# Kernel tuning notes

Hardware: AMD Instinct MI355X
Metric: run time of the kernel (lower is better)

The kernel has to match this reference:

```python
import math
import jax, jax.numpy as jnp
import numpy as np

B, Q, K = 1, 2048, 2048
CQ = CK = CV = 128
H, CH = 8, 32
HD = H * CH  # 256


def setup_inputs() -> dict:
    key = jax.random.key(0)
    ks = jax.random.split(key, 12)
    s = 0.02
    return {
        "q_x": jax.random.normal(ks[0], (B, Q, CQ), jnp.float32),
        "kv_x": jax.random.normal(ks[1], (B, K, CK), jnp.float32),
        "bias": jax.random.normal(ks[2], (B, 1, Q, K), jnp.float32),
        "distance": jax.random.uniform(ks[3], (B, Q, K, H), jnp.float32),
        "Wq": jax.random.normal(ks[4], (CQ, HD), jnp.float32) * s,
        "Wk": jax.random.normal(ks[5], (CK, HD), jnp.float32) * s,
        "Wv": jax.random.normal(ks[6], (CV, HD), jnp.float32) * s,
        "Wg": jax.random.normal(ks[7], (CQ, HD), jnp.float32) * s,
        "bg": jnp.zeros((HD,), jnp.float32),
        "Wo": jax.random.normal(ks[8], (HD, CQ), jnp.float32) * s,
        "bo": jnp.zeros((CQ,), jnp.float32),
    }


def reference(q_x, kv_x, bias, distance, Wq, Wk, Wv, Wg, bg, Wo, bo):
    # Projections -> [B, S, H, CH]
    q = (q_x @ Wq).reshape(B, Q, H, CH) / math.sqrt(CH)
    k = (kv_x @ Wk).reshape(B, K, H, CH)
    v = (kv_x @ Wv).reshape(B, K, H, CH)
    # Scores [B, H, Q, K]
    a = jnp.einsum("bqhc,bkhc->bhqk", q, k)
    a = a + bias
    # mha_permu=True: distance [B,Q,K,H] -> [B,H,Q,K]; rel_dis_pair_bias='add'
    a = a + jnp.transpose(distance, (0, 3, 1, 2))
    a = jax.nn.softmax(a, axis=-1)
    o = jnp.einsum("bhqk,bkhc->bqhc", a, v)  # [B, Q, H, CH]
    # Gating
    g = jax.nn.sigmoid(q_x @ Wg + bg).reshape(B, Q, H, CH)
    o = o * g
    o = o.reshape(B, Q, HD)
    return o @ Wo + bo
```

## Files before the change

### kernel.cpp

```cpp
#include <hip/hip_runtime.h>
#include <hip/hip_bf16.h>

#define Qn 2048
#define Kn 2048
#define Cin 128
#define Hn 8
#define CHn 32
#define HDn 256
#define QK (Qn * Kn)
#define NSPLIT 8

typedef __attribute__((ext_vector_type(8))) short short8;
typedef __attribute__((ext_vector_type(4))) float f32x4;

static __device__ __forceinline__ unsigned short f2bf(float f) {
    unsigned int u = __float_as_uint(f);
    u += 0x7fffu + ((u >> 16) & 1u);
    return (unsigned short)(u >> 16);
}

__global__ __launch_bounds__(256) void proj_kernel(
    const float* __restrict__ qx, const float* __restrict__ kvx,
    const float* __restrict__ Wq, const float* __restrict__ Wk,
    const float* __restrict__ Wv, const float* __restrict__ Wg,
    const float* __restrict__ bg,
    unsigned short* __restrict__ qb, unsigned short* __restrict__ kb,
    unsigned short* __restrict__ vtb, float* __restrict__ gb)
{
    const int mat = blockIdx.y;
    const int r0 = blockIdx.x * 8;
    const int j = threadIdx.x;
    const float* A = (mat == 0 || mat == 3) ? qx : kvx;
    const float* W = (mat == 0) ? Wq : (mat == 1) ? Wk : (mat == 2) ? Wv : Wg;
    const float* Ar = A + r0 * Cin;
    float acc[8] = {0.f, 0.f, 0.f, 0.f, 0.f, 0.f, 0.f, 0.f};
    for (int c = 0; c < Cin; ++c) {
        const float w = W[c * HDn + j];
        #pragma unroll
        for (int i = 0; i < 8; ++i)
            acc[i] = fmaf(Ar[i * Cin + c], w, acc[i]);
    }
    if (mat == 0) {
        const float s = 0.17677669529663687f;
        #pragma unroll
        for (int i = 0; i < 8; ++i)
            qb[(r0 + i) * HDn + j] = f2bf(acc[i] * s);
    } else if (mat == 1) {
        #pragma unroll
        for (int i = 0; i < 8; ++i)
            kb[(r0 + i) * HDn + j] = f2bf(acc[i]);
    } else if (mat == 2) {
        unsigned short tmp[8];
        #pragma unroll
        for (int i = 0; i < 8; ++i) tmp[i] = f2bf(acc[i]);
        *(short8*)(vtb + (size_t)j * Kn + r0) = *(short8*)tmp;
    } else {
        const float b = bg[j];
        #pragma unroll
        for (int i = 0; i < 8; ++i)
            gb[(r0 + i) * HDn + j] = 1.f / (1.f + __expf(-(acc[i] + b)));
    }
}

__global__ __launch_bounds__(256) void prepass_kernel(
    const float* __restrict__ bias, const float* __restrict__ dist,
    _Float16* __restrict__ db)
{
    __shared__ _Float16 lds[Hn * 272];
    const int q = blockIdx.x;
    const int k0 = blockIdx.y * 256;
    const int t = threadIdx.x;
    const float b = bias[q * Kn + k0 + t];
    const float4* dp = (const float4*)(dist + (size_t)(q * Kn + k0 + t) * Hn);
    const float4 d0 = dp[0];
    const float4 d1 = dp[1];
    lds[0 * 272 + t] = (_Float16)(d0.x + b);
    lds[1 * 272 + t] = (_Float16)(d0.y + b);
    lds[2 * 272 + t] = (_Float16)(d0.z + b);
    lds[3 * 272 + t] = (_Float16)(d0.w + b);
    lds[4 * 272 + t] = (_Float16)(d1.x + b);
    lds[5 * 272 + t] = (_Float16)(d1.y + b);
    lds[6 * 272 + t] = (_Float16)(d1.z + b);
    lds[7 * 272 + t] = (_Float16)(d1.w + b);
    __syncthreads();
    const int h = t >> 5;
    const int c8 = (t & 31) * 8;
    const short8 v = *(const short8*)(lds + h * 272 + c8);
    *(short8*)((unsigned short*)db + (size_t)h * QK + (size_t)q * Kn + k0 + c8) = v;
}

template <bool USE_DB>
__global__ __launch_bounds__(512) void attn_kernel(
    const unsigned short* __restrict__ qb, const unsigned short* __restrict__ kb,
    const unsigned short* __restrict__ vtb,
    const _Float16* __restrict__ db,
    const float* __restrict__ bias, const float* __restrict__ dist,
    float* __restrict__ opart, float* __restrict__ lpart)
{
    __shared__ unsigned short ps[Hn][16][72];
    const int bx = blockIdx.x;
    const int qt = bx >> 3;
    const int sp = bx & 7;
    const int q0 = qt * 16;
    const int k00 = sp * 256;
    const int tid = threadIdx.x;
    const int h = tid >> 6;
    const int l = tid & 63;
    const int g = l >> 4;
    const int n = l & 15;

    const short8 qf = *(const short8*)(qb + (q0 + n) * HDn + h * CHn + g * 8);
    const _Float16* dbh = db + (size_t)h * QK;

    f32x4 o0 = {0.f, 0.f, 0.f, 0.f};
    f32x4 o1 = {0.f, 0.f, 0.f, 0.f};
    float lacc[4] = {0.f, 0.f, 0.f, 0.f};
    unsigned short* psh = &ps[h][0][0];
    const f32x4 z = {0.f, 0.f, 0.f, 0.f};

    for (int kt = 0; kt < 4; ++kt) {
        const int k0 = k00 + kt * 64;
        float dbv[4][4];
        #pragma unroll
        for (int kkg = 0; kkg < 4; ++kkg) {
            #pragma unroll
            for (int r = 0; r < 4; ++r) {
                const int qg = q0 + g * 4 + r;
                const int kg = k0 + kkg * 16 + n;
                if (USE_DB)
                    dbv[kkg][r] = (float)dbh[(size_t)qg * Kn + kg];
                else
                    dbv[kkg][r] = bias[(size_t)qg * Kn + kg] +
                                  dist[((size_t)qg * Kn + kg) * Hn + h];
            }
        }
        f32x4 sf[4];
        #pragma unroll
        for (int kkg = 0; kkg < 4; ++kkg) {
            const short8 kf = *(const short8*)(kb + (k0 + kkg * 16 + n) * HDn + h * CHn + g * 8);
            sf[kkg] = __builtin_amdgcn_mfma_f32_16x16x32_bf16(qf, kf, z, 0, 0, 0);
        }
        #pragma unroll
        for (int kkg = 0; kkg < 4; ++kkg) {
            #pragma unroll
            for (int r = 0; r < 4; ++r) {
                const float p = __expf(sf[kkg][r] + dbv[kkg][r]);
                sf[kkg][r] = p;
                lacc[r] += p;
            }
        }
        #pragma unroll
        for (int kkg = 0; kkg < 4; ++kkg) {
            #pragma unroll
            for (int r = 0; r < 4; ++r)
                psh[(g * 4 + r) * 72 + kkg * 16 + n] = f2bf(sf[kkg][r]);
        }
        #pragma unroll
        for (int chunk = 0; chunk < 2; ++chunk) {
            const short8 pf = *(const short8*)(psh + n * 72 + chunk * 32 + g * 8);
            const short8 vf0 = *(const short8*)(vtb + (h * CHn + n) * Kn + k0 + chunk * 32 + g * 8);
            o0 = __builtin_amdgcn_mfma_f32_16x16x32_bf16(pf, vf0, o0, 0, 0, 0);
            const short8 vf1 = *(const short8*)(vtb + (h * CHn + 16 + n) * Kn + k0 + chunk * 32 + g * 8);
            o1 = __builtin_amdgcn_mfma_f32_16x16x32_bf16(pf, vf1, o1, 0, 0, 0);
        }
    }
    float* op = opart + (size_t)sp * (Qn * HDn);
    #pragma unroll
    for (int r = 0; r < 4; ++r) {
        const int qg = q0 + g * 4 + r;
        op[qg * HDn + h * CHn + n] = o0[r];
        op[qg * HDn + h * CHn + 16 + n] = o1[r];
        float v = lacc[r];
        v += __shfl_xor(v, 1);
        v += __shfl_xor(v, 2);
        v += __shfl_xor(v, 4);
        v += __shfl_xor(v, 8);
        lacc[r] = v;
    }
    if (n == 0) {
        float* lp = lpart + (size_t)sp * (Qn * Hn);
        #pragma unroll
        for (int r = 0; r < 4; ++r)
            lp[(q0 + g * 4 + r) * Hn + h] = lacc[r];
    }
}

__global__ __launch_bounds__(256) void mergeout_kernel(
    const float* __restrict__ opart, const float* __restrict__ lpart,
    const float* __restrict__ gb, const float* __restrict__ Wo,
    const float* __restrict__ bo, float* __restrict__ out)
{
    __shared__ float olds[HDn];
    __shared__ float red[4][128];
    const int q = blockIdx.x;
    const int t = threadIdx.x;
    const int h = t >> 5;
    float s = 0.f;
    #pragma unroll
    for (int sp = 0; sp < NSPLIT; ++sp)
        s += opart[(size_t)sp * (Qn * HDn) + q * HDn + t];
    float lt = 0.f;
    #pragma unroll
    for (int sp = 0; sp < NSPLIT; ++sp)
        lt += lpart[(size_t)sp * (Qn * Hn) + q * Hn + h];
    olds[t] = (s / lt) * gb[q * HDn + t];
    __syncthreads();
    const int p = t & 63;
    const int seg = t >> 6;
    float a0 = 0.f, a1 = 0.f;
    for (int c = seg * 64; c < seg * 64 + 64; ++c) {
        const float ov = olds[c];
        const float2 w = *(const float2*)(Wo + c * Cin + 2 * p);
        a0 = fmaf(ov, w.x, a0);
        a1 = fmaf(ov, w.y, a1);
    }
    red[seg][2 * p] = a0;
    red[seg][2 * p + 1] = a1;
    __syncthreads();
    if (t < 128)
        out[q * Cin + t] = red[0][t] + red[1][t] + red[2][t] + red[3][t] + bo[t];
}

extern "C" void kernel_launch(void* const* d_in, const int* in_sizes, int n_in,
                              void* d_out, int out_size, void* d_ws, size_t ws_size,
                              hipStream_t stream)
{
    const float* qx   = (const float*)d_in[0];
    const float* kvx  = (const float*)d_in[1];
    const float* bias = (const float*)d_in[2];
    const float* dist = (const float*)d_in[3];
    const float* Wq   = (const float*)d_in[4];
    const float* Wk   = (const float*)d_in[5];
    const float* Wv   = (const float*)d_in[6];
    const float* Wg   = (const float*)d_in[7];
    const float* bg   = (const float*)d_in[8];
    const float* Wo   = (const float*)d_in[9];
    const float* bo   = (const float*)d_in[10];
    float* out = (float*)d_out;

    char* w = (char*)d_ws;
    unsigned short* qb  = (unsigned short*)(w);
    unsigned short* kb  = (unsigned short*)(w + (1ull << 20));
    unsigned short* vtb = (unsigned short*)(w + (2ull << 20));
    float* gb    = (float*)(w + (3ull << 20));
    float* opart = (float*)(w + (5ull << 20));
    float* lpart = (float*)(w + (21ull << 20));
    _Float16* db = (_Float16*)(w + (22ull << 20));
    const size_t need_db = 86ull << 20;

    proj_kernel<<<dim3(Qn / 8, 4), 256, 0, stream>>>(qx, kvx, Wq, Wk, Wv, Wg, bg, qb, kb, vtb, gb);
    if (ws_size >= need_db) {
        prepass_kernel<<<dim3(Qn, Kn / 256), 256, 0, stream>>>(bias, dist, db);
        attn_kernel<true><<<dim3(128 * NSPLIT), 512, 0, stream>>>(qb, kb, vtb, db, bias, dist, opart, lpart);
    } else {
        attn_kernel<false><<<dim3(128 * NSPLIT), 512, 0, stream>>>(qb, kb, vtb, db, bias, dist, opart, lpart);
    }
    mergeout_kernel<<<dim3(Qn), 256, 0, stream>>>(opart, lpart, gb, Wo, bo, out);
}
```

Measured before the change: 310.6 us.

## Fuse bias+distance prepass into attention kernel via LDS-staged transpose with prefetch

Removes the separate prepass kernel that wrote a per-head fp16 copy of bias+distance to global memory. The attention kernel now loads distance and bias directly with coalesced vector reads, converts to fp16, and transposes them through shared memory. It prefetches the next k-tile's values into registers while the current tile computes. This cuts one full write and read pass over a 64 MB intermediate, at the cost of extra LDS use, two block barriers per tile, and an occupancy hint on the launch bounds.

```diff
diff --git a/kernel.cpp b/kernel.cpp
--- a/kernel.cpp
+++ b/kernel.cpp
@@ -7,8 +7,8 @@
 #define Hn 8
 #define CHn 32
 #define HDn 256
-#define QK (Qn * Kn)
 #define NSPLIT 8
+#define KP 68
 
 typedef __attribute__((ext_vector_type(8))) short short8;
 typedef __attribute__((ext_vector_type(4))) float f32x4;
@@ -62,55 +62,31 @@
     }
 }
 
-__global__ __launch_bounds__(256) void prepass_kernel(
-    const float* __restrict__ bias, const float* __restrict__ dist,
-    _Float16* __restrict__ db)
-{
-    __shared__ _Float16 lds[Hn * 272];
-    const int q = blockIdx.x;
-    const int k0 = blockIdx.y * 256;
-    const int t = threadIdx.x;
-    const float b = bias[q * Kn + k0 + t];
-    const float4* dp = (const float4*)(dist + (size_t)(q * Kn + k0 + t) * Hn);
-    const float4 d0 = dp[0];
-    const float4 d1 = dp[1];
-    lds[0 * 272 + t] = (_Float16)(d0.x + b);
-    lds[1 * 272 + t] = (_Float16)(d0.y + b);
-    lds[2 * 272 + t] = (_Float16)(d0.z + b);
-    lds[3 * 272 + t] = (_Float16)(d0.w + b);
-    lds[4 * 272 + t] = (_Float16)(d1.x + b);
-    lds[5 * 272 + t] = (_Float16)(d1.y + b);
-    lds[6 * 272 + t] = (_Float16)(d1.z + b);
-    lds[7 * 272 + t] = (_Float16)(d1.w + b);
-    __syncthreads();
-    const int h = t >> 5;
-    const int c8 = (t & 31) * 8;
-    const short8 v = *(const short8*)(lds + h * 272 + c8);
-    *(short8*)((unsigned short*)db + (size_t)h * QK + (size_t)q * Kn + k0 + c8) = v;
-}
-
-template <bool USE_DB>
-__global__ __launch_bounds__(512) void attn_kernel(
+__global__ __launch_bounds__(512, 6) void attn_kernel(
     const unsigned short* __restrict__ qb, const unsigned short* __restrict__ kb,
     const unsigned short* __restrict__ vtb,
-    const _Float16* __restrict__ db,
     const float* __restrict__ bias, const float* __restrict__ dist,
     float* __restrict__ opart, float* __restrict__ lpart)
 {
     __shared__ unsigned short ps[Hn][16][72];
+    __shared__ _Float16 dbl[Hn * 16 * KP];
+
     const int bx = blockIdx.x;
     const int qt = bx >> 3;
     const int sp = bx & 7;
     const int q0 = qt * 16;
     const int k00 = sp * 256;
-    const int tid = threadIdx.x;
-    const int h = tid >> 6;
-    const int l = tid & 63;
+    const int t = threadIdx.x;
+    const int h = t >> 6;
+    const int l = t & 63;
     const int g = l >> 4;
     const int n = l & 15;
 
+    const int sk = (t >> 1) & 63;
+    const int shg = t & 1;
+    const int sqb = t >> 7;
+
     const short8 qf = *(const short8*)(qb + (q0 + n) * HDn + h * CHn + g * 8);
-    const _Float16* dbh = db + (size_t)h * QK;
 
     f32x4 o0 = {0.f, 0.f, 0.f, 0.f};
     f32x4 o1 = {0.f, 0.f, 0.f, 0.f};
@@ -118,20 +94,32 @@
     unsigned short* psh = &ps[h][0][0];
     const f32x4 z = {0.f, 0.f, 0.f, 0.f};
 
+    f32x4 dv[4];
+    float bv[4];
+    #pragma unroll
+    for (int i = 0; i < 4; ++i) {
+        const int qi = q0 + sqb + 4 * i;
+        dv[i] = *(const f32x4*)(dist + ((size_t)qi * Kn + k00 + sk) * Hn + 4 * shg);
+        bv[i] = bias[(size_t)qi * Kn + k00 + sk];
+    }
+
     for (int kt = 0; kt < 4; ++kt) {
         const int k0 = k00 + kt * 64;
-        float dbv[4][4];
-        #pragma unroll
-        for (int kkg = 0; kkg < 4; ++kkg) {
-            #pragma unroll
-            for (int r = 0; r < 4; ++r) {
-                const int qg = q0 + g * 4 + r;
-                const int kg = k0 + kkg * 16 + n;
-                if (USE_DB)
-                    dbv[kkg][r] = (float)dbh[(size_t)qg * Kn + kg];
-                else
-                    dbv[kkg][r] = bias[(size_t)qg * Kn + kg] +
-                                  dist[((size_t)qg * Kn + kg) * Hn + h];
+        __syncthreads();
+        #pragma unroll
+        for (int i = 0; i < 4; ++i) {
+            const int qi = sqb + 4 * i;
+            #pragma unroll
+            for (int j = 0; j < 4; ++j)
+                dbl[((shg * 4 + j) * 16 + qi) * KP + sk] = (_Float16)(dv[i][j] + bv[i]);
+        }
+        __syncthreads();
+        if (kt < 3) {
+            #pragma unroll
+            for (int i = 0; i < 4; ++i) {
+                const int qi = q0 + sqb + 4 * i;
+                dv[i] = *(const f32x4*)(dist + ((size_t)qi * Kn + k0 + 64 + sk) * Hn + 4 * shg);
+                bv[i] = bias[(size_t)qi * Kn + k0 + 64 + sk];
             }
         }
         f32x4 sf[4];
@@ -140,11 +128,13 @@
             const short8 kf = *(const short8*)(kb + (k0 + kkg * 16 + n) * HDn + h * CHn + g * 8);
             sf[kkg] = __builtin_amdgcn_mfma_f32_16x16x32_bf16(qf, kf, z, 0, 0, 0);
         }
+        const _Float16* dbh = dbl + h * 16 * KP;
         #pragma unroll
         for (int kkg = 0; kkg < 4; ++kkg) {
             #pragma unroll
             for (int r = 0; r < 4; ++r) {
-                const float p = __expf(sf[kkg][r] + dbv[kkg][r]);
+                const float db = (float)dbh[(g * 4 + r) * KP + kkg * 16 + n];
+                const float p = __expf(sf[kkg][r] + db);
                 sf[kkg][r] = p;
                 lacc[r] += p;
             }
@@ -245,15 +235,8 @@
     float* gb    = (float*)(w + (3ull << 20));
     float* opart = (float*)(w + (5ull << 20));
     float* lpart = (float*)(w + (21ull << 20));
-    _Float16* db = (_Float16*)(w + (22ull << 20));
-    const size_t need_db = 86ull << 20;
 
     proj_kernel<<<dim3(Qn / 8, 4), 256, 0, stream>>>(qx, kvx, Wq, Wk, Wv, Wg, bg, qb, kb, vtb, gb);
-    if (ws_size >= need_db) {
-        prepass_kernel<<<dim3(Qn, Kn / 256), 256, 0, stream>>>(bias, dist, db);
-        attn_kernel<true><<<dim3(128 * NSPLIT), 512, 0, stream>>>(qb, kb, vtb, db, bias, dist, opart, lpart);
-    } else {
-        attn_kernel<false><<<dim3(128 * NSPLIT), 512, 0, stream>>>(qb, kb, vtb, db, bias, dist, opart, lpart);
-    }
+    attn_kernel<<<dim3(128 * NSPLIT), 512, 0, stream>>>(qb, kb, vtb, bias, dist, opart, lpart);
     mergeout_kernel<<<dim3(Qn), 256, 0, stream>>>(opart, lpart, gb, Wo, bo, out);
 }
```

Measured after the change: 281.9 us. 9.2% less time.
